# Optimization experiments

Measured on AMD Instinct MI355X. Metric: run time of the kernel, lower is better.

The kernel has to match this reference:

```python
import math
import jax, jax.numpy as jnp
import numpy as np


def _expmap0(u):
    # geoopt Lorentz (k=1) expmap0 followed by projection back onto the hyperboloid.
    # Minkowski norm of the tangent input (geoopt clamps at 1e-8 before sqrt).
    u0 = u[..., :1]
    us = u[..., 1:]
    mink = -u0 * u0 + jnp.sum(us * us, axis=-1, keepdims=True)
    nomin = jnp.sqrt(jnp.maximum(mink, 1e-8))
    r = jnp.sinh(nomin) * u / nomin
    space = r[..., 1:]
    time = jnp.sqrt(1.0 + jnp.sum(space * space, axis=-1, keepdims=True))  # project()
    return jnp.concatenate([time, space], axis=-1)


def setup_inputs() -> dict:
    key = jax.random.key(0)
    B, T, E, H = 2, 1024, 1024, 16
    ks = jax.random.split(key, 8)
    s = 0.02
    return {
        "x": jax.random.normal(ks[0], (B, T, E), jnp.float32),
        "Wqkv": jax.random.normal(ks[1], (3 * E, E), jnp.float32) * s,
        "bqkv": jnp.zeros((3 * E,), jnp.float32),
        "Wout": jax.random.normal(ks[2], (E, E), jnp.float32) * s,
        "bout": jnp.zeros((E,), jnp.float32),
        "Wimp": jax.random.normal(ks[3], (1, E), jnp.float32) * s,
        "bimp": jnp.zeros((1,), jnp.float32),
        "Walpha": jax.random.normal(ks[4], (H, E), jnp.float32) * s,
        "balpha": jnp.zeros((H,), jnp.float32),
        "spike_threshold": jnp.asarray(0.5, jnp.float32),
        "log_k": jnp.full((H,), 0.54, jnp.float32),
        "qk_scale": jnp.asarray(0.1, jnp.float32),
    }


def reference(x, Wqkv, bqkv, Wout, bout, Wimp, bimp, Walpha, balpha,
              spike_threshold, log_k, qk_scale):
    B, T, C = x.shape
    H = log_k.shape[0]
    D = C // H

    importance = jax.nn.sigmoid(x @ Wimp.T + bimp)          # (B,T,1)
    # torch.tril on the (T,1) trailing dims keeps every element -> no-op mask.
    spikes = (importance > spike_threshold).astype(x.dtype)
    spike_mask = spikes.reshape(B, 1, T, 1)

    alpha = jax.nn.sigmoid(x @ Walpha.T + balpha)           # (B,T,H)
    alpha = jnp.transpose(alpha, (0, 2, 1))[..., None]      # (B,H,T,1)

    qkv = (x @ Wqkv.T + bqkv).reshape(B, T, 3, H, D)
    q = jnp.transpose(qkv[:, :, 0], (0, 2, 1, 3))           # (B,H,T,D)
    k = jnp.transpose(qkv[:, :, 1], (0, 2, 1, 3))
    v = jnp.transpose(qkv[:, :, 2], (0, 2, 1, 3))

    scores_euclid = jnp.einsum('bhtd,bhsd->bhts', q, k) / math.sqrt(D)

    safe_scale = jax.nn.sigmoid(qk_scale) * 1.5
    qn = q / jnp.maximum(jnp.linalg.norm(q, axis=-1, keepdims=True), 1e-12) * safe_scale
    kn = k / jnp.maximum(jnp.linalg.norm(k, axis=-1, keepdims=True), 1e-12) * safe_scale
    q_hyp = _expmap0(qn)
    k_hyp = _expmap0(kn)

    inner = (-jnp.einsum('bhti,bhsi->bhts', q_hyp[..., :1], k_hyp[..., :1])
             + jnp.einsum('bhtd,bhsd->bhts', q_hyp[..., 1:], k_hyp[..., 1:]))
    curv_k = (jax.nn.softplus(log_k) + 1e-6).reshape(1, H, 1, 1)
    mdot = jnp.maximum(-inner, 1.0 + 1e-6)
    dist = jnp.arccosh(mdot)
    scores_hyper = -(dist * dist) / curv_k

    scores = (1.0 - alpha) * scores_euclid + alpha * scores_hyper
    causal = jnp.tril(jnp.ones((T, T), bool))
    scores = jnp.where(causal[None, None], scores, -jnp.inf)

    attn = jax.nn.softmax(scores, axis=-1) * spike_mask     # dropout disabled (eval)
    y = jnp.einsum('bhts,bhsd->bhtd', attn, v)
    y = jnp.transpose(y, (0, 2, 1, 3)).reshape(B, T, C)
    return y @ Wout.T + bout
```

## Files before the change

kernel.cpp:

```cpp
#include <hip/hip_runtime.h>
#include <math.h>

#define B_ 2
#define T_ 1024
#define E_ 1024
#define H_ 16
#define D_ 64
#define M_ (B_*T_)

typedef __bf16 bf16x8 __attribute__((ext_vector_type(8)));
typedef __bf16 bf16x4 __attribute__((ext_vector_type(4)));
typedef float f32x4 __attribute__((ext_vector_type(4)));

__device__ __forceinline__ void* ldsp(__bf16* base, int row, int byte) {
  return (char*)base + row * 128 + (byte ^ ((row & 7) << 4));
}

__device__ __forceinline__ void gload_lds16(const void* g, void* l) {
  __builtin_amdgcn_global_load_lds((const __attribute__((address_space(1))) void*)g,
                                   (__attribute__((address_space(3))) void*)l, 16, 0, 0);
}

#define XV4 524288
#define WQV4 786432
#define WOV4 262144
#define TOTV4 (XV4 + WQV4 + WOV4)
__global__ __launch_bounds__(256) void conv_kernel(
    const float* __restrict__ x, const float* __restrict__ Wqkv,
    const float* __restrict__ Wout,
    __bf16* __restrict__ xb, __bf16* __restrict__ Wqkvb, __bf16* __restrict__ Woutb) {
  for (size_t i = (size_t)blockIdx.x * blockDim.x + threadIdx.x; i < TOTV4;
       i += (size_t)gridDim.x * blockDim.x) {
    const float4* src; __bf16* dst; size_t off;
    if (i < XV4)            { src = (const float4*)x;    dst = xb;    off = i; }
    else if (i < XV4+WQV4)  { src = (const float4*)Wqkv; dst = Wqkvb; off = i - XV4; }
    else                    { src = (const float4*)Wout; dst = Woutb; off = i - XV4 - WQV4; }
    float4 val = src[off];
    bf16x4 o = {(__bf16)val.x, (__bf16)val.y, (__bf16)val.z, (__bf16)val.w};
    *(bf16x4*)(dst + off * 4) = o;
  }
}

__global__ __launch_bounds__(256) void imp_alpha_kernel(
    const float* __restrict__ x,
    const float* __restrict__ Wimp, const float* __restrict__ bimp,
    const float* __restrict__ Walpha, const float* __restrict__ balpha,
    const float* __restrict__ thr_p,
    float* __restrict__ spike, float* __restrict__ alpha) {
  int m = blockIdx.x;
  int tid = threadIdx.x;
  const float* xr = x + (size_t)m * E_;
  float part[17];
#pragma unroll
  for (int i = 0; i < 17; ++i) part[i] = 0.f;
  for (int e = tid; e < E_; e += 256) {
    float xv = xr[e];
    part[16] += xv * Wimp[e];
#pragma unroll
    for (int h = 0; h < 16; ++h) part[h] += xv * Walpha[h * E_ + e];
  }
  __shared__ float red[17][4];
  int lane = tid & 63, wv = tid >> 6;
#pragma unroll
  for (int i = 0; i < 17; ++i) {
    float v = part[i];
    for (int off = 32; off > 0; off >>= 1) v += __shfl_down(v, off, 64);
    if (lane == 0) red[i][wv] = v;
  }
  __syncthreads();
  if (tid < 17) {
    float v = red[tid][0] + red[tid][1] + red[tid][2] + red[tid][3];
    if (tid == 16) {
      float z = v + bimp[0];
      float sig = 1.f / (1.f + expf(-z));
      spike[m] = (sig > thr_p[0]) ? 1.f : 0.f;
    } else {
      float z = v + balpha[tid];
      float a = 1.f / (1.f + expf(-z));
      int b = m >> 10, t = m & (T_ - 1);
      alpha[((size_t)(b * H_ + tid)) * T_ + t] = a;
    }
  }
}

__global__ __launch_bounds__(256) void qkv_gemm_kernel(
    const __bf16* __restrict__ A, const __bf16* __restrict__ Bm,
    const float* __restrict__ bias,
    __bf16* __restrict__ q, __bf16* __restrict__ k, __bf16* __restrict__ v) {
  __shared__ __bf16 As[128 * 32];
  __shared__ __bf16 Bs[128 * 32];
  const int K = E_;
  int tid = threadIdx.x;
  int w = tid >> 6, lane = tid & 63, lr = lane & 15, g = lane >> 4;
  int m0 = blockIdx.y * 128, n0 = blockIdx.x * 128;
  int wr = (w >> 1) * 64, wc = (w & 1) * 64;

  int task0 = tid, task1 = tid + 256;
  int r0s = task0 >> 2, c0s = task0 & 3;
  int r1s = task1 >> 2, c1s = task1 & 3;
  const __bf16* gA0 = A + (size_t)(m0 + r0s) * K + c0s * 8;
  const __bf16* gA1 = A + (size_t)(m0 + r1s) * K + c1s * 8;
  const __bf16* gB0 = Bm + (size_t)(n0 + r0s) * K + c0s * 8;
  const __bf16* gB1 = Bm + (size_t)(n0 + r1s) * K + c1s * 8;
  __bf16* lA0 = As + task0 * 8;
  __bf16* lA1 = As + task1 * 8;
  __bf16* lB0 = Bs + task0 * 8;
  __bf16* lB1 = Bs + task1 * 8;

  f32x4 acc[4][4];
#pragma unroll
  for (int i = 0; i < 4; ++i)
#pragma unroll
    for (int j = 0; j < 4; ++j) acc[i][j] = (f32x4){0.f, 0.f, 0.f, 0.f};

  for (int k0 = 0; k0 < K; k0 += 32) {
    gload_lds16(gA0, lA0); gload_lds16(gA1, lA1);
    gload_lds16(gB0, lB0); gload_lds16(gB1, lB1);
    gA0 += 32; gA1 += 32; gB0 += 32; gB1 += 32;
    __syncthreads();
    bf16x8 af[4], bf[4];
#pragma unroll
    for (int i = 0; i < 4; ++i) af[i] = *(bf16x8*)&As[(wr + i * 16 + lr) * 32 + g * 8];
#pragma unroll
    for (int j = 0; j < 4; ++j) bf[j] = *(bf16x8*)&Bs[(wc + j * 16 + lr) * 32 + g * 8];
#pragma unroll
    for (int i = 0; i < 4; ++i)
#pragma unroll
      for (int j = 0; j < 4; ++j)
        acc[i][j] = __builtin_amdgcn_mfma_f32_16x16x32_bf16(af[i], bf[j], acc[i][j], 0, 0, 0);
    __syncthreads();
  }

#pragma unroll
  for (int i = 0; i < 4; ++i) {
#pragma unroll
    for (int r = 0; r < 4; ++r) {
      int m = m0 + wr + i * 16 + g * 4 + r;
      int b = m >> 10, t = m & (T_ - 1);
#pragma unroll
      for (int j = 0; j < 4; ++j) {
        int n = n0 + wc + j * 16 + lr;
        float val = acc[i][j][r] + bias[n];
        int comp = n >> 10, h = (n >> 6) & 15, d = n & 63;
        __bf16* dst = (comp == 0) ? q : ((comp == 1) ? k : v);
        dst[(((size_t)(b * H_ + h)) * T_ + t) * 64 + d] = (__bf16)val;
      }
    }
  }
}

__global__ __launch_bounds__(256) void hyp_kernel(
    const __bf16* __restrict__ q, const __bf16* __restrict__ k,
    const float* __restrict__ qk_scale_p,
    __bf16* __restrict__ qh, __bf16* __restrict__ khn) {
  int wid = blockIdx.x * 4 + (threadIdx.x >> 6);
  int lane = threadIdx.x & 63;
  int is_k = wid >> 15;
  int row = wid & 32767;
  const __bf16* src = (is_k ? k : q) + (size_t)row * 64;
  float u = (float)src[lane];
  float nsq = u * u;
#pragma unroll
  for (int off = 32; off > 0; off >>= 1) nsq += __shfl_xor(nsq, off, 64);
  float norm = fmaxf(sqrtf(nsq), 1e-12f);
  float ss = 1.5f / (1.f + expf(-qk_scale_p[0]));
  float un = u / norm * ss;
  float s2 = un * un;
  float tot = s2;
#pragma unroll
  for (int off = 32; off > 0; off >>= 1) tot += __shfl_xor(tot, off, 64);
  float un0 = __shfl(un, 0, 64);
  float mink = tot - 2.f * un0 * un0;
  float nomin = sqrtf(fmaxf(mink, 1e-8f));
  float sc = sinhf(nomin) / nomin;
  float r = sc * un;
  float sp2 = (lane == 0) ? 0.f : r * r;
  float sps = sp2;
#pragma unroll
  for (int off = 32; off > 0; off >>= 1) sps += __shfl_xor(sps, off, 64);
  float tm = sqrtf(1.f + sps);
  float outv = (lane == 0) ? tm : r;
  if (is_k && lane != 0) outv = -outv;
  (is_k ? khn : qh)[(size_t)row * 64 + lane] = (__bf16)outv;
}

__global__ __launch_bounds__(256) void vtr_kernel(
    const __bf16* __restrict__ v, __bf16* __restrict__ vt) {
  __shared__ __bf16 tile[64][65];
  int bh = blockIdx.x >> 4;
  int s0 = (blockIdx.x & 15) * 64;
  int tid = threadIdx.x;
#pragma unroll
  for (int it = 0; it < 2; ++it) {
    int task = tid + it * 256;
    int r = task >> 3, c = (task & 7) * 8;
    bf16x8 a = *(const bf16x8*)(v + ((size_t)bh * T_ + s0 + r) * 64 + c);
#pragma unroll
    for (int i = 0; i < 8; ++i) tile[r][c + i] = a[i];
  }
  __syncthreads();
#pragma unroll
  for (int it = 0; it < 2; ++it) {
    int task = tid + it * 256;
    int dd = task >> 3, sc = (task & 7) * 8;
    bf16x8 o;
#pragma unroll
    for (int i = 0; i < 8; ++i) o[i] = tile[sc + i][dd];
    *(bf16x8*)(vt + ((size_t)bh * 64 + dd) * T_ + s0 + sc) = o;
  }
}

__global__ __launch_bounds__(256) void attn_kernel(
    const __bf16* __restrict__ q, const __bf16* __restrict__ k,
    const __bf16* __restrict__ qh, const __bf16* __restrict__ khn,
    const __bf16* __restrict__ vt,
    const float* __restrict__ alpha, const float* __restrict__ log_k,
    __bf16* __restrict__ pacc, float* __restrict__ pml) {
  __shared__ __bf16 pslab_all[4][16 * 64];
  int tid = threadIdx.x;
  int w = tid >> 6, lane = tid & 63;
  int wid = blockIdx.x * 4 + w;
  int bh = wid & 31;
  int rest = wid >> 5;
  int half = rest & 1;
  int qt = rest >> 1;
  int h = bh & 15;
  int lr = lane & 15, g = lane >> 4;
  int n_st = (qt >> 2) + 1;
  const size_t base = (size_t)bh * T_ * 64;
  const size_t vtb = (size_t)bh * 64 * T_;
  __bf16* pslab = pslab_all[w];

  const __bf16* qrow = q + base + (size_t)(qt * 16 + lr) * 64;
  const __bf16* qhrow = qh + base + (size_t)(qt * 16 + lr) * 64;
  bf16x8 aq0 = *(const bf16x8*)(qrow + g * 8);
  bf16x8 aq1 = *(const bf16x8*)(qrow + 32 + g * 8);
  bf16x8 ah0 = *(const bf16x8*)(qhrow + g * 8);
  bf16x8 ah1 = *(const bf16x8*)(qhrow + 32 + g * 8);

  float curv = log1pf(expf(log_k[h])) + 1e-6f;
  float hc = 0.69314718056f / curv;
  const float ec = 0.18033688f;
  int tg[4]; float al[4];
#pragma unroll
  for (int r = 0; r < 4; ++r) {
    tg[r] = qt * 16 + g * 4 + r;
    al[r] = alpha[(size_t)bh * T_ + tg[r]];
  }

  float m_r[4] = {-1e30f, -1e30f, -1e30f, -1e30f};
  float l_r[4] = {0.f, 0.f, 0.f, 0.f};
  f32x4 acc[4];
#pragma unroll
  for (int n = 0; n < 4; ++n) acc[n] = (f32x4){0.f, 0.f, 0.f, 0.f};

  for (int st = half; st < n_st; st += 2) {
    int s0 = st * 64;
    bool diag = (st == n_st - 1);
    float pv[4][4];
    float pmax[4] = {-1e30f, -1e30f, -1e30f, -1e30f};
#pragma unroll
    for (int j = 0; j < 4; ++j) {
      if (diag && (s0 + j * 16 > qt * 16 + 15)) {
#pragma unroll
        for (int r = 0; r < 4; ++r) pv[j][r] = -1e30f;
        continue;
      }
      const __bf16* kr = k + base + (size_t)(s0 + j * 16 + lr) * 64;
      const __bf16* khr = khn + base + (size_t)(s0 + j * 16 + lr) * 64;
      bf16x8 bk0 = *(const bf16x8*)(kr + g * 8);
      bf16x8 bk1 = *(const bf16x8*)(kr + 32 + g * 8);
      f32x4 z = {0.f, 0.f, 0.f, 0.f};
      z = __builtin_amdgcn_mfma_f32_16x16x32_bf16(aq0, bk0, z, 0, 0, 0);
      f32x4 se = __builtin_amdgcn_mfma_f32_16x16x32_bf16(aq1, bk1, z, 0, 0, 0);
      bf16x8 bh0 = *(const bf16x8*)(khr + g * 8);
      bf16x8 bh1 = *(const bf16x8*)(khr + 32 + g * 8);
      f32x4 z2 = {0.f, 0.f, 0.f, 0.f};
      z2 = __builtin_amdgcn_mfma_f32_16x16x32_bf16(ah0, bh0, z2, 0, 0, 0);
      f32x4 sh = __builtin_amdgcn_mfma_f32_16x16x32_bf16(ah1, bh1, z2, 0, 0, 0);
      int sg = s0 + j * 16 + lr;
#pragma unroll
      for (int r = 0; r < 4; ++r) {
        float sc_e = se[r] * ec;
        float md = fmaxf(sh[r], 1.0f + 1e-6f);
        float l2 = __log2f(md + sqrtf(fmaf(md, md, -1.f)));
        float t = fmaf(l2 * l2, hc, sc_e);
        float s = fmaf(-al[r], t, sc_e);
        if (diag && sg > tg[r]) s = -1e30f;
        pv[j][r] = s;
        pmax[r] = fmaxf(pmax[r], s);
      }
    }
#pragma unroll
    for (int r = 0; r < 4; ++r) {
      float mx = pmax[r];
      mx = fmaxf(mx, __shfl_xor(mx, 1, 64));
      mx = fmaxf(mx, __shfl_xor(mx, 2, 64));
      mx = fmaxf(mx, __shfl_xor(mx, 4, 64));
      mx = fmaxf(mx, __shfl_xor(mx, 8, 64));
      float mn = fmaxf(m_r[r], mx);
      float fac = exp2f(m_r[r] - mn);
      m_r[r] = mn;
      float ls = 0.f;
#pragma unroll
      for (int j = 0; j < 4; ++j) { pv[j][r] = exp2f(pv[j][r] - mn); ls += pv[j][r]; }
      ls += __shfl_xor(ls, 1, 64);
      ls += __shfl_xor(ls, 2, 64);
      ls += __shfl_xor(ls, 4, 64);
      ls += __shfl_xor(ls, 8, 64);
      l_r[r] = l_r[r] * fac + ls;
#pragma unroll
      for (int n = 0; n < 4; ++n) acc[n][r] *= fac;
    }
#pragma unroll
    for (int j = 0; j < 4; ++j)
#pragma unroll
      for (int r = 0; r < 4; ++r)
        *(__bf16*)ldsp(pslab, g * 4 + r, (j * 16 + lr) * 2) = (__bf16)pv[j][r];
    bf16x8 ap0 = *(bf16x8*)ldsp(pslab, lr, g * 16);
    bf16x8 ap1 = *(bf16x8*)ldsp(pslab, lr, 64 + g * 16);
#pragma unroll
    for (int n = 0; n < 4; ++n) {
      const __bf16* vr = vt + vtb + (size_t)(n * 16 + lr) * T_ + s0;
      bf16x8 bv0 = *(const bf16x8*)(vr + g * 8);
      bf16x8 bv1 = *(const bf16x8*)(vr + 32 + g * 8);
      acc[n] = __builtin_amdgcn_mfma_f32_16x16x32_bf16(ap0, bv0, acc[n], 0, 0, 0);
      acc[n] = __builtin_amdgcn_mfma_f32_16x16x32_bf16(ap1, bv1, acc[n], 0, 0, 0);
    }
  }

  int pidx = ((bh << 6) + qt) * 2 + half;
  __bf16* pa = pacc + (size_t)pidx * 1024;
#pragma unroll
  for (int n = 0; n < 4; ++n)
#pragma unroll
    for (int r = 0; r < 4; ++r)
      pa[(g * 4 + r) * 64 + n * 16 + lr] = (__bf16)acc[n][r];
  if (lr == 0) {
#pragma unroll
    for (int r = 0; r < 4; ++r) {
      pml[(size_t)pidx * 32 + g * 4 + r] = m_r[r];
      pml[(size_t)pidx * 32 + 16 + g * 4 + r] = l_r[r];
    }
  }
}

__global__ __launch_bounds__(256) void merge_kernel(
    const __bf16* __restrict__ pacc, const float* __restrict__ pml,
    const float* __restrict__ spike, __bf16* __restrict__ yw) {
  int tid = threadIdx.x;
  int w = tid >> 6, lane = tid & 63;
  int wid = blockIdx.x * 4 + w;
  int bh = wid & 31;
  int qt = wid >> 5;
  int b = bh >> 4, h = bh & 15;
  size_t i1 = ((size_t)(bh << 6) + qt) * 2;
  size_t i2 = i1 + 1;
  const __bf16* a1 = pacc + i1 * 1024;
  const __bf16* a2 = pacc + i2 * 1024;
#pragma unroll 4
  for (int row = 0; row < 16; ++row) {
    float m1 = pml[i1 * 32 + row], l1 = pml[i1 * 32 + 16 + row];
    float m2 = pml[i2 * 32 + row], l2 = pml[i2 * 32 + 16 + row];
    float mm = fmaxf(m1, m2);
    float f1 = exp2f(m1 - mm), f2 = exp2f(m2 - mm);
    float l = l1 * f1 + l2 * f2;
    int t = qt * 16 + row;
    float iv = spike[(size_t)b * T_ + t] / l;
    float val = ((float)a1[row * 64 + lane] * f1 +
                 (float)a2[row * 64 + lane] * f2) * iv;
    yw[(size_t)(b * T_ + t) * E_ + h * 64 + lane] = (__bf16)val;
  }
}

__global__ __launch_bounds__(256) void out_gemm_kernel(
    const __bf16* __restrict__ A, const __bf16* __restrict__ Bm,
    const float* __restrict__ bias, float* __restrict__ outp) {
  __shared__ __bf16 As[128 * 32];
  __shared__ __bf16 Bs[128 * 32];
  const int K = E_;
  int tid = threadIdx.x;
  int w = tid >> 6, lane = tid & 63, lr = lane & 15, g = lane >> 4;
  int m0 = blockIdx.y * 128, n0 = blockIdx.x * 128;
  int wr = (w >> 1) * 64, wc = (w & 1) * 64;

  int task0 = tid, task1 = tid + 256;
  int r0s = task0 >> 2, c0s = task0 & 3;
  int r1s = task1 >> 2, c1s = task1 & 3;
  const __bf16* gA0 = A + (size_t)(m0 + r0s) * K + c0s * 8;
  const __bf16* gA1 = A + (size_t)(m0 + r1s) * K + c1s * 8;
  const __bf16* gB0 = Bm + (size_t)(n0 + r0s) * K + c0s * 8;
  const __bf16* gB1 = Bm + (size_t)(n0 + r1s) * K + c1s * 8;
  __bf16* lA0 = As + task0 * 8;
  __bf16* lA1 = As + task1 * 8;
  __bf16* lB0 = Bs + task0 * 8;
  __bf16* lB1 = Bs + task1 * 8;

  f32x4 acc[4][4];
#pragma unroll
  for (int i = 0; i < 4; ++i)
#pragma unroll
    for (int j = 0; j < 4; ++j) acc[i][j] = (f32x4){0.f, 0.f, 0.f, 0.f};

  for (int k0 = 0; k0 < K; k0 += 32) {
    gload_lds16(gA0, lA0); gload_lds16(gA1, lA1);
    gload_lds16(gB0, lB0); gload_lds16(gB1, lB1);
    gA0 += 32; gA1 += 32; gB0 += 32; gB1 += 32;
    __syncthreads();
    bf16x8 af[4], bf[4];
#pragma unroll
    for (int i = 0; i < 4; ++i) af[i] = *(bf16x8*)&As[(wr + i * 16 + lr) * 32 + g * 8];
#pragma unroll
    for (int j = 0; j < 4; ++j) bf[j] = *(bf16x8*)&Bs[(wc + j * 16 + lr) * 32 + g * 8];
#pragma unroll
    for (int i = 0; i < 4; ++i)
#pragma unroll
      for (int j = 0; j < 4; ++j)
        acc[i][j] = __builtin_amdgcn_mfma_f32_16x16x32_bf16(af[i], bf[j], acc[i][j], 0, 0, 0);
    __syncthreads();
  }

#pragma unroll
  for (int i = 0; i < 4; ++i) {
#pragma unroll
    for (int r = 0; r < 4; ++r) {
      int m = m0 + wr + i * 16 + g * 4 + r;
#pragma unroll
      for (int j = 0; j < 4; ++j) {
        int n = n0 + wc + j * 16 + lr;
        outp[(size_t)m * E_ + n] = acc[i][j][r] + bias[n];
      }
    }
  }
}

extern "C" void kernel_launch(void* const* d_in, const int* in_sizes, int n_in,
                              void* d_out, int out_size, void* d_ws, size_t ws_size,
                              hipStream_t stream) {
  const float* x      = (const float*)d_in[0];
  const float* Wqkv   = (const float*)d_in[1];
  const float* bqkv   = (const float*)d_in[2];
  const float* Wout   = (const float*)d_in[3];
  const float* bout   = (const float*)d_in[4];
  const float* Wimp   = (const float*)d_in[5];
  const float* bimp   = (const float*)d_in[6];
  const float* Walpha = (const float*)d_in[7];
  const float* balpha = (const float*)d_in[8];
  const float* thr    = (const float*)d_in[9];
  const float* log_k  = (const float*)d_in[10];
  const float* qk_sc  = (const float*)d_in[11];
  float* out = (float*)d_out;

  char* ws = (char*)d_ws;
  size_t off = 0;
  auto alloc = [&](size_t bytes) -> void* {
    void* p = (void*)(ws + off);
    off += (bytes + 255) & ~(size_t)255;
    return p;
  };
  const size_t qkv_elems = (size_t)B_ * H_ * T_ * D_;
  __bf16* xb    = (__bf16*)alloc((size_t)M_ * E_ * 2);
  __bf16* Wqkvb = (__bf16*)alloc((size_t)3 * E_ * E_ * 2);
  __bf16* Woutb = (__bf16*)alloc((size_t)E_ * E_ * 2);
  __bf16* q   = (__bf16*)alloc(qkv_elems * 2);
  __bf16* k   = (__bf16*)alloc(qkv_elems * 2);
  __bf16* v   = (__bf16*)alloc(qkv_elems * 2);
  __bf16* qh  = (__bf16*)alloc(qkv_elems * 2);
  __bf16* khn = (__bf16*)alloc(qkv_elems * 2);
  __bf16* vt  = (__bf16*)alloc(qkv_elems * 2);
  __bf16* yw  = (__bf16*)alloc((size_t)M_ * E_ * 2);
  float* alphaw = (float*)alloc((size_t)B_ * H_ * T_ * sizeof(float));
  float* spikew = (float*)alloc((size_t)M_ * sizeof(float));
  float* pml    = (float*)alloc((size_t)4096 * 32 * sizeof(float));
  __bf16* pacc = (__bf16*)ws;

  conv_kernel<<<1024, 256, 0, stream>>>(x, Wqkv, Wout, xb, Wqkvb, Woutb);
  imp_alpha_kernel<<<M_, 256, 0, stream>>>(x, Wimp, bimp, Walpha, balpha, thr,
                                           spikew, alphaw);
  qkv_gemm_kernel<<<dim3(24, 16), 256, 0, stream>>>(xb, Wqkvb, bqkv, q, k, v);
  hyp_kernel<<<(2 * B_ * H_ * T_) / 4, 256, 0, stream>>>(q, k, qk_sc, qh, khn);
  vtr_kernel<<<B_ * H_ * (T_ / 64), 256, 0, stream>>>(v, vt);
  attn_kernel<<<1024, 256, 0, stream>>>(q, k, qh, khn, vt, alphaw, log_k,
                                        pacc, pml);
  merge_kernel<<<512, 256, 0, stream>>>(pacc, pml, spikew, yw);
  out_gemm_kernel<<<dim3(8, 16), 256, 0, stream>>>(yw, Woutb, bout, out);
}
```

Baseline: 183.4 us.

## Share K/Kh/V tiles in LDS across waves and fuse V transpose into attention

Each block now handles a 64-row query tile with four waves that share K, hyperbolic K and a transposed V tile staged in LDS, instead of every wave reading K/V from global memory on its own. The separate V transpose kernel is removed and the transpose happens while V is written to LDS. The key range is split into two contiguous halves rather than interleaved, and block-to-head mapping is reordered. In exchange it adds two block barriers per key tile, scalar LDS stores for the transpose, and coarser work units that may worsen load balance across the causal triangle.

Measured after the change: 153.0 us. -16.6%, faster.

```diff
diff --git a/kernel.cpp b/kernel.cpp
--- a/kernel.cpp
+++ b/kernel.cpp
@@ -184,55 +184,36 @@
   (is_k ? khn : qh)[(size_t)row * 64 + lane] = (__bf16)outv;
 }
 
-__global__ __launch_bounds__(256) void vtr_kernel(
-    const __bf16* __restrict__ v, __bf16* __restrict__ vt) {
-  __shared__ __bf16 tile[64][65];
-  int bh = blockIdx.x >> 4;
-  int s0 = (blockIdx.x & 15) * 64;
-  int tid = threadIdx.x;
-#pragma unroll
-  for (int it = 0; it < 2; ++it) {
-    int task = tid + it * 256;
-    int r = task >> 3, c = (task & 7) * 8;
-    bf16x8 a = *(const bf16x8*)(v + ((size_t)bh * T_ + s0 + r) * 64 + c);
-#pragma unroll
-    for (int i = 0; i < 8; ++i) tile[r][c + i] = a[i];
-  }
-  __syncthreads();
-#pragma unroll
-  for (int it = 0; it < 2; ++it) {
-    int task = tid + it * 256;
-    int dd = task >> 3, sc = (task & 7) * 8;
-    bf16x8 o;
-#pragma unroll
-    for (int i = 0; i < 8; ++i) o[i] = tile[sc + i][dd];
-    *(bf16x8*)(vt + ((size_t)bh * 64 + dd) * T_ + s0 + sc) = o;
-  }
-}
-
 __global__ __launch_bounds__(256) void attn_kernel(
-    const __bf16* __restrict__ q, const __bf16* __restrict__ k,
+    const __bf16* __restrict__ q, const __bf16* __restrict__ k, const __bf16* __restrict__ v,
     const __bf16* __restrict__ qh, const __bf16* __restrict__ khn,
-    const __bf16* __restrict__ vt,
     const float* __restrict__ alpha, const float* __restrict__ log_k,
     __bf16* __restrict__ pacc, float* __restrict__ pml) {
-  __shared__ __bf16 pslab_all[4][16 * 64];
+  __shared__ __bf16 k_s[64 * 64];
+  __shared__ __bf16 kh_s[64 * 64];
+  __shared__ __bf16 vt_s[64 * 64];
+  __shared__ __bf16 p_s[64 * 64];
+
+  int bid = blockIdx.x;
+  int bh = ((bid & 7) << 2) | ((bid >> 3) & 3);
+  int rest = bid >> 5;
+  int qt = rest & 15;
+  int half = rest >> 4;
+  int h = bh & 15;
+  int t0 = qt * 64;
+  int n_st = qt + 1;
+  int nh = (n_st + 1) >> 1;
+  int s_beg = half ? nh : 0;
+  int s_end = half ? n_st : nh;
+
   int tid = threadIdx.x;
   int w = tid >> 6, lane = tid & 63;
-  int wid = blockIdx.x * 4 + w;
-  int bh = wid & 31;
-  int rest = wid >> 5;
-  int half = rest & 1;
-  int qt = rest >> 1;
-  int h = bh & 15;
   int lr = lane & 15, g = lane >> 4;
-  int n_st = (qt >> 2) + 1;
+  int trow = w * 16;
   const size_t base = (size_t)bh * T_ * 64;
-  const size_t vtb = (size_t)bh * 64 * T_;
-  __bf16* pslab = pslab_all[w];
-
-  const __bf16* qrow = q + base + (size_t)(qt * 16 + lr) * 64;
-  const __bf16* qhrow = qh + base + (size_t)(qt * 16 + lr) * 64;
+
+  const __bf16* qrow = q + base + (size_t)(t0 + trow + lr) * 64;
+  const __bf16* qhrow = qh + base + (size_t)(t0 + trow + lr) * 64;
   bf16x8 aq0 = *(const bf16x8*)(qrow + g * 8);
   bf16x8 aq1 = *(const bf16x8*)(qrow + 32 + g * 8);
   bf16x8 ah0 = *(const bf16x8*)(qhrow + g * 8);
@@ -244,7 +225,7 @@
   int tg[4]; float al[4];
 #pragma unroll
   for (int r = 0; r < 4; ++r) {
-    tg[r] = qt * 16 + g * 4 + r;
+    tg[r] = t0 + trow + g * 4 + r;
     al[r] = alpha[(size_t)bh * T_ + tg[r]];
   }
 
@@ -254,27 +235,46 @@
 #pragma unroll
   for (int n = 0; n < 4; ++n) acc[n] = (f32x4){0.f, 0.f, 0.f, 0.f};
 
-  for (int st = half; st < n_st; st += 2) {
+  for (int st = s_beg; st < s_end; ++st) {
     int s0 = st * 64;
     bool diag = (st == n_st - 1);
+    __syncthreads();
+#pragma unroll
+    for (int it = 0; it < 2; ++it) {
+      int task = tid + it * 256;
+      int row = task >> 3, cj = task & 7;
+      bf16x8 a = *(const bf16x8*)(k + base + (size_t)(s0 + row) * 64 + cj * 8);
+      bf16x8 c = *(const bf16x8*)(khn + base + (size_t)(s0 + row) * 64 + cj * 8);
+      *(bf16x8*)ldsp(k_s, row, cj * 16) = a;
+      *(bf16x8*)ldsp(kh_s, row, cj * 16) = c;
+    }
+#pragma unroll
+    for (int it = 0; it < 2; ++it) {
+      int task = tid + it * 256;
+      int srow = task & 63, dc = task >> 6;
+      bf16x8 a = *(const bf16x8*)(v + base + (size_t)(s0 + srow) * 64 + dc * 8);
+#pragma unroll
+      for (int i = 0; i < 8; ++i)
+        *(__bf16*)ldsp(vt_s, dc * 8 + i, srow * 2) = a[i];
+    }
+    __syncthreads();
+
     float pv[4][4];
     float pmax[4] = {-1e30f, -1e30f, -1e30f, -1e30f};
 #pragma unroll
     for (int j = 0; j < 4; ++j) {
-      if (diag && (s0 + j * 16 > qt * 16 + 15)) {
+      if (diag && (s0 + j * 16 > t0 + trow + 15)) {
 #pragma unroll
         for (int r = 0; r < 4; ++r) pv[j][r] = -1e30f;
         continue;
       }
-      const __bf16* kr = k + base + (size_t)(s0 + j * 16 + lr) * 64;
-      const __bf16* khr = khn + base + (size_t)(s0 + j * 16 + lr) * 64;
-      bf16x8 bk0 = *(const bf16x8*)(kr + g * 8);
-      bf16x8 bk1 = *(const bf16x8*)(kr + 32 + g * 8);
+      bf16x8 bk0 = *(bf16x8*)ldsp(k_s, j * 16 + lr, g * 16);
+      bf16x8 bk1 = *(bf16x8*)ldsp(k_s, j * 16 + lr, 64 + g * 16);
       f32x4 z = {0.f, 0.f, 0.f, 0.f};
       z = __builtin_amdgcn_mfma_f32_16x16x32_bf16(aq0, bk0, z, 0, 0, 0);
       f32x4 se = __builtin_amdgcn_mfma_f32_16x16x32_bf16(aq1, bk1, z, 0, 0, 0);
-      bf16x8 bh0 = *(const bf16x8*)(khr + g * 8);
-      bf16x8 bh1 = *(const bf16x8*)(khr + 32 + g * 8);
+      bf16x8 bh0 = *(bf16x8*)ldsp(kh_s, j * 16 + lr, g * 16);
+      bf16x8 bh1 = *(bf16x8*)ldsp(kh_s, j * 16 + lr, 64 + g * 16);
       f32x4 z2 = {0.f, 0.f, 0.f, 0.f};
       z2 = __builtin_amdgcn_mfma_f32_16x16x32_bf16(ah0, bh0, z2, 0, 0, 0);
       f32x4 sh = __builtin_amdgcn_mfma_f32_16x16x32_bf16(ah1, bh1, z2, 0, 0, 0);
@@ -316,20 +316,20 @@
     for (int j = 0; j < 4; ++j)
 #pragma unroll
       for (int r = 0; r < 4; ++r)
-        *(__bf16*)ldsp(pslab, g * 4 + r, (j * 16 + lr) * 2) = (__bf16)pv[j][r];
-    bf16x8 ap0 = *(bf16x8*)ldsp(pslab, lr, g * 16);
-    bf16x8 ap1 = *(bf16x8*)ldsp(pslab, lr, 64 + g * 16);
+        *(__bf16*)ldsp(p_s, trow + g * 4 + r, (j * 16 + lr) * 2) = (__bf16)pv[j][r];
+    bf16x8 ap0 = *(bf16x8*)ldsp(p_s, trow + lr, g * 16);
+    bf16x8 ap1 = *(bf16x8*)ldsp(p_s, trow + lr, 64 + g * 16);
 #pragma unroll
     for (int n = 0; n < 4; ++n) {
-      const __bf16* vr = vt + vtb + (size_t)(n * 16 + lr) * T_ + s0;
-      bf16x8 bv0 = *(const bf16x8*)(vr + g * 8);
-      bf16x8 bv1 = *(const bf16x8*)(vr + 32 + g * 8);
+      bf16x8 bv0 = *(bf16x8*)ldsp(vt_s, n * 16 + lr, g * 16);
+      bf16x8 bv1 = *(bf16x8*)ldsp(vt_s, n * 16 + lr, 64 + g * 16);
       acc[n] = __builtin_amdgcn_mfma_f32_16x16x32_bf16(ap0, bv0, acc[n], 0, 0, 0);
       acc[n] = __builtin_amdgcn_mfma_f32_16x16x32_bf16(ap1, bv1, acc[n], 0, 0, 0);
     }
   }
 
-  int pidx = ((bh << 6) + qt) * 2 + half;
+  int qt16 = (qt << 2) | w;
+  int pidx = ((bh << 6) + qt16) * 2 + half;
   __bf16* pa = pacc + (size_t)pidx * 1024;
 #pragma unroll
   for (int n = 0; n < 4; ++n)
@@ -467,7 +467,6 @@
   __bf16* v   = (__bf16*)alloc(qkv_elems * 2);
   __bf16* qh  = (__bf16*)alloc(qkv_elems * 2);
   __bf16* khn = (__bf16*)alloc(qkv_elems * 2);
-  __bf16* vt  = (__bf16*)alloc(qkv_elems * 2);
   __bf16* yw  = (__bf16*)alloc((size_t)M_ * E_ * 2);
   float* alphaw = (float*)alloc((size_t)B_ * H_ * T_ * sizeof(float));
   float* spikew = (float*)alloc((size_t)M_ * sizeof(float));
@@ -479,8 +478,7 @@
                                            spikew, alphaw);
   qkv_gemm_kernel<<<dim3(24, 16), 256, 0, stream>>>(xb, Wqkvb, bqkv, q, k, v);
   hyp_kernel<<<(2 * B_ * H_ * T_) / 4, 256, 0, stream>>>(q, k, qk_sc, qh, khn);
-  vtr_kernel<<<B_ * H_ * (T_ / 64), 256, 0, stream>>>(v, vt);
-  attn_kernel<<<1024, 256, 0, stream>>>(q, k, qh, khn, vt, alphaw, log_k,
+  attn_kernel<<<1024, 256, 0, stream>>>(q, k, v, qh, khn, alphaw, log_k,
                                         pacc, pml);
   merge_kernel<<<512, 256, 0, stream>>>(pacc, pml, spikew, yw);
   out_gemm_kernel<<<dim3(8, 16), 256, 0, stream>>>(yw, Woutb, bout, out);
```
